# Kernel optimization log

Measured on AMD Instinct MI355X. Metric: run time of the kernel, lower is better.

The kernel has to match this reference:

```python
import jax, jax.numpy as jnp
import numpy as np

DIM = 512
NUM_HEADS = 8
DIM_HEAD = 64
EPS = 1e-8
ROPE_THETA = 10000.0


def rms_norm(x, gamma):
    # F.normalize(x, dim=-1, p=2, eps) * sqrt(dim) * gamma
    norm = jnp.sqrt(jnp.sum(x * x, axis=-1, keepdims=True))
    x = x / jnp.maximum(norm, EPS)
    return x * (DIM ** 0.5) * gamma


def apply_rope(x):
    # x: [b, h, n, d], interleaved-pair RoPE (rotary-embedding-torch style)
    n, d = x.shape[-2], x.shape[-1]
    inv_freq = 1.0 / (ROPE_THETA ** (jnp.arange(0, d, 2, dtype=jnp.float32) / d))
    freqs = jnp.arange(n, dtype=jnp.float32)[:, None] * inv_freq[None, :]  # [n, d/2]
    freqs = jnp.repeat(freqs, 2, axis=-1)  # [n, d]
    cos, sin = jnp.cos(freqs), jnp.sin(freqs)
    x1 = x[..., ::2]
    x2 = x[..., 1::2]
    rot = jnp.stack((-x2, x1), axis=-1).reshape(x.shape)
    return x * cos + rot * sin


def setup_inputs() -> dict:
    key = jax.random.key(0)
    k1, k2, k3, k4 = jax.random.split(key, 4)
    b, n = 4, 2048
    dim_inner = NUM_HEADS * DIM_HEAD
    x = jax.random.normal(k1, (b, n, DIM), dtype=jnp.float32)
    gamma = jnp.ones((DIM,), dtype=jnp.float32)
    w_qkv = jax.random.normal(k2, (DIM, 3 * dim_inner), dtype=jnp.float32) * (DIM ** -0.5)
    w_out = jax.random.normal(k3, (dim_inner, DIM), dtype=jnp.float32) * (dim_inner ** -0.5)
    return {"x": x, "gamma": gamma, "w_qkv": w_qkv, "w_out": w_out}


def reference(x, gamma, w_qkv, w_out):
    b, n, _ = x.shape
    h, d = NUM_HEADS, DIM_HEAD
    xn = rms_norm(x, gamma)
    qkv = xn @ w_qkv  # [b, n, 3*h*d]
    qkv = qkv.reshape(b, n, 3, h, d)
    q = jnp.transpose(qkv[:, :, 0], (0, 2, 1, 3))  # [b, h, n, d]
    k = jnp.transpose(qkv[:, :, 1], (0, 2, 1, 3))
    v = jnp.transpose(qkv[:, :, 2], (0, 2, 1, 3))
    q = apply_rope(q)
    k = apply_rope(k)
    scale = d ** -0.5
    attn = jnp.einsum('bhnd,bhmd->bhnm', q, k) * scale
    attn = jax.nn.softmax(attn, axis=-1)
    out = jnp.einsum('bhnm,bhmd->bhnd', attn, v)
    out = jnp.transpose(out, (0, 2, 1, 3)).reshape(b, n, h * d)
    return out @ w_out
```

## Files before the change

### kernel.cpp

```cpp
#include <hip/hip_runtime.h>
#include <hip/hip_bf16.h>
#include <cmath>

#define B_SZ 4
#define N_SEQ 2048
#define DIM 512
#define NH 8
#define DH 64
#define QKV_N 1536
#define ROWS (B_SZ * N_SEQ)

typedef __bf16 bf16x8 __attribute__((ext_vector_type(8)));
typedef __bf16 bf16x4 __attribute__((ext_vector_type(4)));
typedef float  f32x4  __attribute__((ext_vector_type(4)));

#define GLOAD_LDS16(gp, lp)                                                     \
    __builtin_amdgcn_global_load_lds(                                           \
        (const __attribute__((address_space(1))) void*)(gp),                    \
        (__attribute__((address_space(3))) void*)(lp), 16, 0, 0)

#define MFMA_BF16 __builtin_amdgcn_mfma_f32_16x16x32_bf16

__global__ __launch_bounds__(64) void rmscast_kernel(const float* __restrict__ x,
                                                     const float* __restrict__ gamma,
                                                     __bf16* __restrict__ A) {
    int row = blockIdx.x;
    int t = threadIdx.x;
    const float4* xr = (const float4*)(x + (size_t)row * DIM);
    float4 a = xr[t];
    float4 b = xr[t + 64];
    float ss = a.x*a.x + a.y*a.y + a.z*a.z + a.w*a.w
             + b.x*b.x + b.y*b.y + b.z*b.z + b.w*b.w;
    #pragma unroll
    for (int off = 32; off > 0; off >>= 1) ss += __shfl_xor(ss, off, 64);
    float s = 22.62741699796952f / fmaxf(sqrtf(ss), 1e-8f);
    const float4* gr = (const float4*)gamma;
    float4 g1 = gr[t], g2 = gr[t + 64];
    bf16x4 o1 = { (__bf16)(a.x*g1.x*s), (__bf16)(a.y*g1.y*s),
                  (__bf16)(a.z*g1.z*s), (__bf16)(a.w*g1.w*s) };
    bf16x4 o2 = { (__bf16)(b.x*g2.x*s), (__bf16)(b.y*g2.y*s),
                  (__bf16)(b.z*g2.z*s), (__bf16)(b.w*g2.w*s) };
    *(bf16x4*)(A + (size_t)row * DIM + t * 4)       = o1;
    *(bf16x4*)(A + (size_t)row * DIM + 256 + t * 4) = o2;
}

__global__ __launch_bounds__(256) void tcast_kernel(const float* __restrict__ W,
                                                    __bf16* __restrict__ Wt,
                                                    int K, int N) {
    __shared__ float Ls[64][68];
    const int n0 = blockIdx.x * 64, k0 = blockIdx.y * 64;
    const int t = threadIdx.x, tx = t & 15, ty = t >> 4;
    #pragma unroll
    for (int i = 0; i < 4; i++) {
        int k = ty + i * 16;
        float4 v = *(const float4*)&W[(size_t)(k0 + k) * N + n0 + tx * 4];
        *(float4*)&Ls[k][tx * 4] = v;
    }
    __syncthreads();
    const int nrow = t >> 2, seg = (t & 3) * 16;
    bf16x8 o0, o1;
    #pragma unroll
    for (int j = 0; j < 8; j++) o0[j] = (__bf16)Ls[seg + j][nrow];
    #pragma unroll
    for (int j = 0; j < 8; j++) o1[j] = (__bf16)Ls[seg + 8 + j][nrow];
    *(bf16x8*)&Wt[(size_t)(n0 + nrow) * K + k0 + seg]     = o0;
    *(bf16x8*)&Wt[(size_t)(n0 + nrow) * K + k0 + seg + 8] = o1;
}

template <int N, typename OutT>
__global__ __launch_bounds__(256) void gemm_bf16_kernel(const __bf16* __restrict__ A,
                                                        const __bf16* __restrict__ Bt,
                                                        OutT* __restrict__ C) {
    __shared__ __bf16 As[128 * 32];
    __shared__ __bf16 Bs[128 * 32];
    const int t = threadIdx.x;
    const int lane = t & 63;
    const int w = t >> 6;
    const int l16 = lane & 15, quad = lane >> 4;
    const int wr = w >> 1, wc = w & 1;
    const int row0 = blockIdx.y * 128, col0 = blockIdx.x * 128;

    f32x4 acc[4][4] = {};

    const int r0a = t >> 2,         ks0 = (t & 3) * 8;
    const int r1a = (t + 256) >> 2, ks1 = (t & 3) * 8;

    for (int kt = 0; kt < DIM; kt += 32) {
        __syncthreads();
        GLOAD_LDS16(A  + (size_t)(row0 + r0a) * DIM + kt + ks0, As + t * 8);
        GLOAD_LDS16(A  + (size_t)(row0 + r1a) * DIM + kt + ks1, As + (t + 256) * 8);
        GLOAD_LDS16(Bt + (size_t)(col0 + r0a) * DIM + kt + ks0, Bs + t * 8);
        GLOAD_LDS16(Bt + (size_t)(col0 + r1a) * DIM + kt + ks1, Bs + (t + 256) * 8);
        __syncthreads();
        bf16x8 af[4], bfr[4];
        #pragma unroll
        for (int mi = 0; mi < 4; mi++)
            af[mi] = *(const bf16x8*)(As + (wr * 64 + mi * 16 + l16) * 32 + quad * 8);
        #pragma unroll
        for (int ni = 0; ni < 4; ni++)
            bfr[ni] = *(const bf16x8*)(Bs + (wc * 64 + ni * 16 + l16) * 32 + quad * 8);
        #pragma unroll
        for (int mi = 0; mi < 4; mi++)
            #pragma unroll
            for (int ni = 0; ni < 4; ni++)
                acc[mi][ni] = MFMA_BF16(af[mi], bfr[ni], acc[mi][ni], 0, 0, 0);
    }
    #pragma unroll
    for (int mi = 0; mi < 4; mi++) {
        #pragma unroll
        for (int ni = 0; ni < 4; ni++) {
            #pragma unroll
            for (int r = 0; r < 4; r++) {
                int m = row0 + wr * 64 + mi * 16 + quad * 4 + r;
                int n = col0 + wc * 64 + ni * 16 + l16;
                if constexpr (sizeof(OutT) == 4) {
                    C[(size_t)m * N + n] = acc[mi][ni][r];
                } else {
                    C[(size_t)m * N + n] = (__bf16)acc[mi][ni][r];
                }
            }
        }
    }
}

__global__ __launch_bounds__(256) void prep_kernel(const __bf16* __restrict__ qkvb,
                                                   __bf16* __restrict__ Qb,
                                                   __bf16* __restrict__ Kf,
                                                   __bf16* __restrict__ Vf) {
    const int bx = blockIdx.x;
    const int nt = bx & 31;
    const int bh = bx >> 5;
    const int b  = bh >> 3;
    const int h  = bh & 7;
    const int t  = threadIdx.x;

    {
        const int r  = t >> 2;
        const int d0 = (t & 3) << 4;
        const int pos = nt * 64 + r;
        const __bf16* qp = qkvb + (size_t)(b * N_SEQ + pos) * QKV_N + h * DH + d0;

        union Pack { __bf16 h[16]; uint4 u[2]; };
        Pack qi, ki, qo, ko;
        qi.u[0] = ((const uint4*)qp)[0];         qi.u[1] = ((const uint4*)qp)[1];
        ki.u[0] = ((const uint4*)(qp + 512))[0]; ki.u[1] = ((const uint4*)(qp + 512))[1];

        #pragma unroll
        for (int i = 0; i < 8; i++) {
            int p = (d0 >> 1) + i;
            float inv = exp2f(-0.41524101186092028f * (float)p);
            float ang = (float)pos * inv;
            float sn, cs;
            sincosf(ang, &sn, &cs);
            float qe = (float)qi.h[2*i], qd = (float)qi.h[2*i+1];
            float ke = (float)ki.h[2*i], kd = (float)ki.h[2*i+1];
            qo.h[2*i]   = (__bf16)(0.125f * (qe * cs - qd * sn));
            qo.h[2*i+1] = (__bf16)(0.125f * (qd * cs + qe * sn));
            ko.h[2*i]   = (__bf16)(ke * cs - kd * sn);
            ko.h[2*i+1] = (__bf16)(kd * cs + ke * sn);
        }
        uint4* qd_ = (uint4*)(Qb + ((size_t)bh * N_SEQ + pos) * DH + d0);
        qd_[0] = qo.u[0]; qd_[1] = qo.u[1];
        const int group = r >> 4, kl = r & 15;
        const int c = d0 >> 5, quad = (d0 & 31) >> 3;
        __bf16* kdst = Kf + ((size_t)bh * 32 + nt) * 4096
                          + (group * 2 + c) * 512 + (quad * 16 + kl) * 8;
        *(uint4*)kdst         = ko.u[0];
        *(uint4*)(kdst + 128) = ko.u[1];
    }

    {
        const int w = t >> 6, lane = t & 63;
        union Pack { __bf16 h[16]; uint4 u[2]; };
        Pack v;
        #pragma unroll
        for (int j = 0; j < 16; j++) {
            int row = nt * 64 + w * 16 + j;
            v.h[j] = qkvb[(size_t)(b * N_SEQ + row) * QKV_N + 1024 + h * DH + lane];
        }
        const int ng = lane >> 4, vl = lane & 15;
        __bf16* vdst = Vf + ((size_t)bh * 32 + nt) * 4096
                          + (ng * 2 + (w >> 1)) * 512 + (((w & 1) * 2) * 16 + vl) * 8;
        *(uint4*)vdst         = v.u[0];
        *(uint4*)(vdst + 128) = v.u[1];
    }
}

__global__ __launch_bounds__(256, 2) void attn_mfma_kernel(const __bf16* __restrict__ Qb,
                                                           const __bf16* __restrict__ Kf,
                                                           const __bf16* __restrict__ Vf,
                                                           __bf16* __restrict__ attn) {
    __shared__ __bf16 kv[2][8192];
    __shared__ __bf16 plds[4][2][16][68];

    const int t    = threadIdx.x;
    const int w    = t >> 6;
    const int lane = t & 63;
    const int l16  = lane & 15;
    const int quad = lane >> 4;

    const int bx = blockIdx.x;
    const int bh = bx & 31;
    const int qc = bx >> 5;
    const int b  = bh >> 3;
    const int h  = bh & 7;

    const int qrow = qc * 128 + w * 32;
    const __bf16* Qh = Qb + ((size_t)bh * N_SEQ + qrow) * DH;
    const __bf16* Kt = Kf + (size_t)bh * 32 * 4096;
    const __bf16* Vt = Vf + (size_t)bh * 32 * 4096;

    bf16x8 qa[2][2];
    #pragma unroll
    for (int f = 0; f < 2; f++) {
        qa[f][0] = *(const bf16x8*)(Qh + (size_t)(f * 16 + l16) * DH + quad * 8);
        qa[f][1] = *(const bf16x8*)(Qh + (size_t)(f * 16 + l16) * DH + 32 + quad * 8);
    }

    bf16x8 ones;
    #pragma unroll
    for (int i = 0; i < 8; i++) ones[i] = (__bf16)1.0f;

    f32x4 O[2][4] = {};
    f32x4 L[2] = {};

    auto dma_tile = [&](int tt, int bb) {
        const __bf16* ks = Kt + (size_t)tt * 4096;
        const __bf16* vs = Vt + (size_t)tt * 4096;
        GLOAD_LDS16(ks + w * 512 + lane * 8,       &kv[bb][w * 512 + lane * 8]);
        GLOAD_LDS16(ks + (w + 4) * 512 + lane * 8, &kv[bb][(w + 4) * 512 + lane * 8]);
        GLOAD_LDS16(vs + w * 512 + lane * 8,       &kv[bb][4096 + w * 512 + lane * 8]);
        GLOAD_LDS16(vs + (w + 4) * 512 + lane * 8, &kv[bb][4096 + (w + 4) * 512 + lane * 8]);
    };

    dma_tile(0, 0);
    for (int tt = 0; tt < 32; tt++) {
        const int cur = tt & 1;
        __syncthreads();
        if (tt + 1 < 32) {
            dma_tile(tt + 1, cur ^ 1);
            asm volatile("s_waitcnt vmcnt(4)" ::: "memory");
        } else {
            asm volatile("s_waitcnt vmcnt(0)" ::: "memory");
        }
        __syncthreads();

        const __bf16* kb = kv[cur];
        const __bf16* vb = kv[cur] + 4096;

        bf16x8 kf[4][2];
        #pragma unroll
        for (int g = 0; g < 4; g++)
            #pragma unroll
            for (int c = 0; c < 2; c++)
                kf[g][c] = *(const bf16x8*)(kb + (g * 2 + c) * 512 + lane * 8);
        bf16x8 vf[4][2];
        #pragma unroll
        for (int n = 0; n < 4; n++)
            #pragma unroll
            for (int kc = 0; kc < 2; kc++)
                vf[n][kc] = *(const bf16x8*)(vb + (n * 2 + kc) * 512 + lane * 8);

        #pragma unroll
        for (int f = 0; f < 2; f++) {
            f32x4 S[4];
            #pragma unroll
            for (int g = 0; g < 4; g++) {
                f32x4 z = {0, 0, 0, 0};
                z = MFMA_BF16(qa[f][0], kf[g][0], z, 0, 0, 0);
                z = MFMA_BF16(qa[f][1], kf[g][1], z, 0, 0, 0);
                S[g] = z;
            }
            #pragma unroll
            for (int g = 0; g < 4; g++)
                #pragma unroll
                for (int r = 0; r < 4; r++)
                    plds[w][f][quad * 4 + r][g * 16 + l16] = (__bf16)__expf(S[g][r]);
        }
        asm volatile("s_waitcnt lgkmcnt(0)" ::: "memory");
        #pragma unroll
        for (int f = 0; f < 2; f++) {
            bf16x8 pa0 = *(const bf16x8*)&plds[w][f][l16][quad * 8];
            bf16x8 pa1 = *(const bf16x8*)&plds[w][f][l16][32 + quad * 8];
            #pragma unroll
            for (int n = 0; n < 4; n++) {
                O[f][n] = MFMA_BF16(pa0, vf[n][0], O[f][n], 0, 0, 0);
                O[f][n] = MFMA_BF16(pa1, vf[n][1], O[f][n], 0, 0, 0);
            }
            L[f] = MFMA_BF16(pa0, ones, L[f], 0, 0, 0);
            L[f] = MFMA_BF16(pa1, ones, L[f], 0, 0, 0);
        }
    }

    #pragma unroll
    for (int f = 0; f < 2; f++) {
        float inv[4];
        #pragma unroll
        for (int r = 0; r < 4; r++) inv[r] = 1.0f / L[f][r];
        #pragma unroll
        for (int n = 0; n < 4; n++)
            #pragma unroll
            for (int r = 0; r < 4; r++) {
                size_t row = (size_t)(b * N_SEQ + qrow + f * 16 + quad * 4 + r);
                attn[row * 512 + h * DH + n * 16 + l16] = (__bf16)(O[f][n][r] * inv[r]);
            }
    }
}

extern "C" void kernel_launch(void* const* d_in, const int* in_sizes, int n_in,
                              void* d_out, int out_size, void* d_ws, size_t ws_size,
                              hipStream_t stream) {
    const float* x     = (const float*)d_in[0];
    const float* gamma = (const float*)d_in[1];
    const float* w_qkv = (const float*)d_in[2];
    const float* w_out = (const float*)d_in[3];
    float* out = (float*)d_out;

    __bf16* Abf   = (__bf16*)d_ws;
    __bf16* Wqkvt = Abf + (size_t)ROWS * DIM;
    __bf16* Woutt = Wqkvt + (size_t)QKV_N * DIM;
    __bf16* qkvb  = Woutt + (size_t)DIM * DIM;
    __bf16* attnb = qkvb;
    __bf16* Qb    = qkvb + (size_t)ROWS * QKV_N;
    __bf16* Kf    = Qb + (size_t)NH * B_SZ * N_SEQ * DH;
    __bf16* Vf    = Kf + (size_t)NH * B_SZ * N_SEQ * DH;

    rmscast_kernel<<<ROWS, 64, 0, stream>>>(x, gamma, Abf);
    tcast_kernel<<<dim3(QKV_N / 64, DIM / 64), 256, 0, stream>>>(w_qkv, Wqkvt, DIM, QKV_N);
    tcast_kernel<<<dim3(DIM / 64, DIM / 64), 256, 0, stream>>>(w_out, Woutt, DIM, DIM);
    gemm_bf16_kernel<QKV_N, __bf16><<<dim3(QKV_N / 128, ROWS / 128), 256, 0, stream>>>(
        Abf, Wqkvt, qkvb);
    prep_kernel<<<1024, 256, 0, stream>>>(qkvb, Qb, Kf, Vf);
    attn_mfma_kernel<<<512, 256, 0, stream>>>(Qb, Kf, Vf, attnb);
    gemm_bf16_kernel<DIM, float><<<dim3(DIM / 128, ROWS / 128), 256, 0, stream>>>(
        attnb, Woutt, out);
}
```

Baseline: 179.9 us.

## Split attention KV range across two blocks with atomic fp32 reduction

Each attention block now processes half of the key/value tiles, doubling the grid to 1024 blocks. Partial unnormalized outputs and row sums are combined with fp32 atomicAdd into zeroed buffers, and a new normalize kernel writes the bf16 result. The launch-bounds occupancy hint goes from 2 to 3 blocks per CU. RoPE cos/sin values are precomputed into a table by a small kernel instead of calling sincos inside prep. This trades better CU fill for extra memsets, atomic traffic, a 16MB fp32 intermediate and an extra kernel launch.

```diff
diff --git a/kernel.cpp b/kernel.cpp
--- a/kernel.cpp
+++ b/kernel.cpp
@@ -20,6 +20,15 @@
         (__attribute__((address_space(3))) void*)(lp), 16, 0, 0)
 
 #define MFMA_BF16 __builtin_amdgcn_mfma_f32_16x16x32_bf16
+
+__global__ __launch_bounds__(256) void cs_kernel(float2* __restrict__ cs) {
+    int idx = blockIdx.x * 256 + threadIdx.x;
+    int pos = idx >> 5, p = idx & 31;
+    float ang = (float)pos * exp2f(-0.41524101186092028f * (float)p);
+    float sn, c;
+    sincosf(ang, &sn, &c);
+    cs[idx] = make_float2(c, sn);
+}
 
 __global__ __launch_bounds__(64) void rmscast_kernel(const float* __restrict__ x,
                                                      const float* __restrict__ gamma,
@@ -124,6 +133,7 @@
 }
 
 __global__ __launch_bounds__(256) void prep_kernel(const __bf16* __restrict__ qkvb,
+                                                   const float2* __restrict__ cstab,
                                                    __bf16* __restrict__ Qb,
                                                    __bf16* __restrict__ Kf,
                                                    __bf16* __restrict__ Vf) {
@@ -145,13 +155,11 @@
         qi.u[0] = ((const uint4*)qp)[0];         qi.u[1] = ((const uint4*)qp)[1];
         ki.u[0] = ((const uint4*)(qp + 512))[0]; ki.u[1] = ((const uint4*)(qp + 512))[1];
 
+        const float2* cse = cstab + (size_t)pos * 32 + (t & 3) * 8;
         #pragma unroll
         for (int i = 0; i < 8; i++) {
-            int p = (d0 >> 1) + i;
-            float inv = exp2f(-0.41524101186092028f * (float)p);
-            float ang = (float)pos * inv;
-            float sn, cs;
-            sincosf(ang, &sn, &cs);
+            float2 csv = cse[i];
+            float cs = csv.x, sn = csv.y;
             float qe = (float)qi.h[2*i], qd = (float)qi.h[2*i+1];
             float ke = (float)ki.h[2*i], kd = (float)ki.h[2*i+1];
             qo.h[2*i]   = (__bf16)(0.125f * (qe * cs - qd * sn));
@@ -186,10 +194,11 @@
     }
 }
 
-__global__ __launch_bounds__(256, 2) void attn_mfma_kernel(const __bf16* __restrict__ Qb,
+__global__ __launch_bounds__(256, 3) void attn_mfma_kernel(const __bf16* __restrict__ Qb,
                                                            const __bf16* __restrict__ Kf,
                                                            const __bf16* __restrict__ Vf,
-                                                           __bf16* __restrict__ attn) {
+                                                           float* __restrict__ Opart,
+                                                           float* __restrict__ Lb) {
     __shared__ __bf16 kv[2][8192];
     __shared__ __bf16 plds[4][2][16][68];
 
@@ -201,14 +210,15 @@
 
     const int bx = blockIdx.x;
     const int bh = bx & 31;
-    const int qc = bx >> 5;
+    const int ks = (bx >> 5) & 1;
+    const int qc = bx >> 6;
     const int b  = bh >> 3;
     const int h  = bh & 7;
 
     const int qrow = qc * 128 + w * 32;
     const __bf16* Qh = Qb + ((size_t)bh * N_SEQ + qrow) * DH;
-    const __bf16* Kt = Kf + (size_t)bh * 32 * 4096;
-    const __bf16* Vt = Vf + (size_t)bh * 32 * 4096;
+    const __bf16* Kt = Kf + ((size_t)bh * 32 + ks * 16) * 4096;
+    const __bf16* Vt = Vf + ((size_t)bh * 32 + ks * 16) * 4096;
 
     bf16x8 qa[2][2];
     #pragma unroll
@@ -225,19 +235,19 @@
     f32x4 L[2] = {};
 
     auto dma_tile = [&](int tt, int bb) {
-        const __bf16* ks = Kt + (size_t)tt * 4096;
-        const __bf16* vs = Vt + (size_t)tt * 4096;
-        GLOAD_LDS16(ks + w * 512 + lane * 8,       &kv[bb][w * 512 + lane * 8]);
-        GLOAD_LDS16(ks + (w + 4) * 512 + lane * 8, &kv[bb][(w + 4) * 512 + lane * 8]);
-        GLOAD_LDS16(vs + w * 512 + lane * 8,       &kv[bb][4096 + w * 512 + lane * 8]);
-        GLOAD_LDS16(vs + (w + 4) * 512 + lane * 8, &kv[bb][4096 + (w + 4) * 512 + lane * 8]);
+        const __bf16* kss = Kt + (size_t)tt * 4096;
+        const __bf16* vss = Vt + (size_t)tt * 4096;
+        GLOAD_LDS16(kss + w * 512 + lane * 8,       &kv[bb][w * 512 + lane * 8]);
+        GLOAD_LDS16(kss + (w + 4) * 512 + lane * 8, &kv[bb][(w + 4) * 512 + lane * 8]);
+        GLOAD_LDS16(vss + w * 512 + lane * 8,       &kv[bb][4096 + w * 512 + lane * 8]);
+        GLOAD_LDS16(vss + (w + 4) * 512 + lane * 8, &kv[bb][4096 + (w + 4) * 512 + lane * 8]);
     };
 
     dma_tile(0, 0);
-    for (int tt = 0; tt < 32; tt++) {
+    for (int tt = 0; tt < 16; tt++) {
         const int cur = tt & 1;
         __syncthreads();
-        if (tt + 1 < 32) {
+        if (tt + 1 < 16) {
             dma_tile(tt + 1, cur ^ 1);
             asm volatile("s_waitcnt vmcnt(4)" ::: "memory");
         } else {
@@ -294,17 +304,30 @@
 
     #pragma unroll
     for (int f = 0; f < 2; f++) {
-        float inv[4];
-        #pragma unroll
-        for (int r = 0; r < 4; r++) inv[r] = 1.0f / L[f][r];
-        #pragma unroll
-        for (int n = 0; n < 4; n++)
-            #pragma unroll
-            for (int r = 0; r < 4; r++) {
-                size_t row = (size_t)(b * N_SEQ + qrow + f * 16 + quad * 4 + r);
-                attn[row * 512 + h * DH + n * 16 + l16] = (__bf16)(O[f][n][r] * inv[r]);
-            }
-    }
+        #pragma unroll
+        for (int r = 0; r < 4; r++) {
+            size_t row = (size_t)(b * N_SEQ + qrow + f * 16 + quad * 4 + r);
+            #pragma unroll
+            for (int n = 0; n < 4; n++)
+                atomicAdd(&Opart[row * 512 + h * DH + n * 16 + l16], O[f][n][r]);
+            if (l16 == 0)
+                atomicAdd(&Lb[(size_t)bh * N_SEQ + qrow + f * 16 + quad * 4 + r], L[f][r]);
+        }
+    }
+}
+
+__global__ __launch_bounds__(256) void norm_kernel(const float* __restrict__ Opart,
+                                                   const float* __restrict__ Lb,
+                                                   __bf16* __restrict__ attnb) {
+    int idx = blockIdx.x * 256 + threadIdx.x;
+    int row = idx >> 7, c4 = idx & 127;
+    int h = c4 >> 4;
+    float l = Lb[(size_t)(((row >> 11) << 3) + h) * N_SEQ + (row & (N_SEQ - 1))];
+    float inv = 1.0f / l;
+    float4 o = ((const float4*)Opart)[idx];
+    bf16x4 ob = { (__bf16)(o.x * inv), (__bf16)(o.y * inv),
+                  (__bf16)(o.z * inv), (__bf16)(o.w * inv) };
+    *(bf16x4*)(attnb + (size_t)idx * 4) = ob;
 }
 
 extern "C" void kernel_launch(void* const* d_in, const int* in_sizes, int n_in,
@@ -320,18 +343,26 @@
     __bf16* Wqkvt = Abf + (size_t)ROWS * DIM;
     __bf16* Woutt = Wqkvt + (size_t)QKV_N * DIM;
     __bf16* qkvb  = Woutt + (size_t)DIM * DIM;
-    __bf16* attnb = qkvb;
+    float*  Opart = (float*)qkvb;
+    float*  Lb    = Opart + (size_t)ROWS * 512;
+    __bf16* attnb = Abf;
     __bf16* Qb    = qkvb + (size_t)ROWS * QKV_N;
     __bf16* Kf    = Qb + (size_t)NH * B_SZ * N_SEQ * DH;
     __bf16* Vf    = Kf + (size_t)NH * B_SZ * N_SEQ * DH;
-
+    float2* cstab = (float2*)(Vf + (size_t)NH * B_SZ * N_SEQ * DH);
+
+    cs_kernel<<<256, 256, 0, stream>>>(cstab);
     rmscast_kernel<<<ROWS, 64, 0, stream>>>(x, gamma, Abf);
     tcast_kernel<<<dim3(QKV_N / 64, DIM / 64), 256, 0, stream>>>(w_qkv, Wqkvt, DIM, QKV_N);
     tcast_kernel<<<dim3(DIM / 64, DIM / 64), 256, 0, stream>>>(w_out, Woutt, DIM, DIM);
     gemm_bf16_kernel<QKV_N, __bf16><<<dim3(QKV_N / 128, ROWS / 128), 256, 0, stream>>>(
         Abf, Wqkvt, qkvb);
-    prep_kernel<<<1024, 256, 0, stream>>>(qkvb, Qb, Kf, Vf);
-    attn_mfma_kernel<<<512, 256, 0, stream>>>(Qb, Kf, Vf, attnb);
+    prep_kernel<<<1024, 256, 0, stream>>>(qkvb, cstab, Qb, Kf, Vf);
+    hipMemsetAsync(Opart, 0, ((size_t)ROWS * 512 + ROWS * NH / 2) * sizeof(float) + 0,
+                   stream);
+    hipMemsetAsync(Lb, 0, (size_t)NH * B_SZ * N_SEQ * sizeof(float), stream);
+    attn_mfma_kernel<<<1024, 256, 0, stream>>>(Qb, Kf, Vf, Opart, Lb);
+    norm_kernel<<<ROWS * 128 / 256, 256, 0, stream>>>(Opart, Lb, attnb);
     gemm_bf16_kernel<DIM, float><<<dim3(DIM / 128, ROWS / 128), 256, 0, stream>>>(
         attnb, Woutt, out);
 }
```

Result: slower. 211.6 us (+17.6%).

## Triple-buffer attention K/V tiles, fold log2e into Q scale, merge weight casts

Applied to the files above, without the earlier changes.

The attention loop moves from double to triple buffering of the K/V LDS tiles. It prefetches two tiles ahead and uses a single waitcnt-plus-barrier per iteration instead of two __syncthreads, which cuts synchronisation stalls and hides global-to-LDS latency. The Q scale now folds in log2(e), so the softmax can use exp2f directly instead of __expf. The two weight transpose-cast launches are merged into one kernel to save a launch. The extra K/V buffer raises LDS use per block, which may limit occupancy under the launch bound of 2 blocks.

```diff
diff --git a/kernel.cpp b/kernel.cpp
--- a/kernel.cpp
+++ b/kernel.cpp
@@ -44,12 +44,11 @@
     *(bf16x4*)(A + (size_t)row * DIM + 256 + t * 4) = o2;
 }
 
-__global__ __launch_bounds__(256) void tcast_kernel(const float* __restrict__ W,
-                                                    __bf16* __restrict__ Wt,
-                                                    int K, int N) {
-    __shared__ float Ls[64][68];
-    const int n0 = blockIdx.x * 64, k0 = blockIdx.y * 64;
-    const int t = threadIdx.x, tx = t & 15, ty = t >> 4;
+__device__ __forceinline__ void tcast_tile(const float* __restrict__ W,
+                                           __bf16* __restrict__ Wt,
+                                           int K, int N, int n0, int k0, int t,
+                                           float (*Ls)[68]) {
+    const int tx = t & 15, ty = t >> 4;
     #pragma unroll
     for (int i = 0; i < 4; i++) {
         int k = ty + i * 16;
@@ -65,6 +64,16 @@
     for (int j = 0; j < 8; j++) o1[j] = (__bf16)Ls[seg + 8 + j][nrow];
     *(bf16x8*)&Wt[(size_t)(n0 + nrow) * K + k0 + seg]     = o0;
     *(bf16x8*)&Wt[(size_t)(n0 + nrow) * K + k0 + seg + 8] = o1;
+}
+
+__global__ __launch_bounds__(256) void tcast2_kernel(const float* __restrict__ w_qkv,
+                                                     const float* __restrict__ w_out,
+                                                     __bf16* __restrict__ Wqkvt,
+                                                     __bf16* __restrict__ Woutt) {
+    __shared__ float Ls[64][68];
+    const int bx = blockIdx.x, k0 = blockIdx.y * 64, t = threadIdx.x;
+    if (bx < 24) tcast_tile(w_qkv, Wqkvt, DIM, QKV_N, bx * 64, k0, t, Ls);
+    else         tcast_tile(w_out, Woutt, DIM, DIM, (bx - 24) * 64, k0, t, Ls);
 }
 
 template <int N, typename OutT>
@@ -133,6 +142,7 @@
     const int b  = bh >> 3;
     const int h  = bh & 7;
     const int t  = threadIdx.x;
+    const float QSCALE = 0.18033688011112042f;
 
     {
         const int r  = t >> 2;
@@ -154,8 +164,8 @@
             sincosf(ang, &sn, &cs);
             float qe = (float)qi.h[2*i], qd = (float)qi.h[2*i+1];
             float ke = (float)ki.h[2*i], kd = (float)ki.h[2*i+1];
-            qo.h[2*i]   = (__bf16)(0.125f * (qe * cs - qd * sn));
-            qo.h[2*i+1] = (__bf16)(0.125f * (qd * cs + qe * sn));
+            qo.h[2*i]   = (__bf16)(QSCALE * (qe * cs - qd * sn));
+            qo.h[2*i+1] = (__bf16)(QSCALE * (qd * cs + qe * sn));
             ko.h[2*i]   = (__bf16)(ke * cs - kd * sn);
             ko.h[2*i+1] = (__bf16)(kd * cs + ke * sn);
         }
@@ -190,7 +200,7 @@
                                                            const __bf16* __restrict__ Kf,
                                                            const __bf16* __restrict__ Vf,
                                                            __bf16* __restrict__ attn) {
-    __shared__ __bf16 kv[2][8192];
+    __shared__ __bf16 kv[3][8192];
     __shared__ __bf16 plds[4][2][16][68];
 
     const int t    = threadIdx.x;
@@ -225,25 +235,27 @@
     f32x4 L[2] = {};
 
     auto dma_tile = [&](int tt, int bb) {
-        const __bf16* ks = Kt + (size_t)tt * 4096;
-        const __bf16* vs = Vt + (size_t)tt * 4096;
-        GLOAD_LDS16(ks + w * 512 + lane * 8,       &kv[bb][w * 512 + lane * 8]);
-        GLOAD_LDS16(ks + (w + 4) * 512 + lane * 8, &kv[bb][(w + 4) * 512 + lane * 8]);
-        GLOAD_LDS16(vs + w * 512 + lane * 8,       &kv[bb][4096 + w * 512 + lane * 8]);
-        GLOAD_LDS16(vs + (w + 4) * 512 + lane * 8, &kv[bb][4096 + (w + 4) * 512 + lane * 8]);
+        const __bf16* kss = Kt + (size_t)tt * 4096;
+        const __bf16* vss = Vt + (size_t)tt * 4096;
+        GLOAD_LDS16(kss + w * 512 + lane * 8,       &kv[bb][w * 512 + lane * 8]);
+        GLOAD_LDS16(kss + (w + 4) * 512 + lane * 8, &kv[bb][(w + 4) * 512 + lane * 8]);
+        GLOAD_LDS16(vss + w * 512 + lane * 8,       &kv[bb][4096 + w * 512 + lane * 8]);
+        GLOAD_LDS16(vss + (w + 4) * 512 + lane * 8, &kv[bb][4096 + (w + 4) * 512 + lane * 8]);
     };
 
     dma_tile(0, 0);
+    dma_tile(1, 1);
+    int cur = 0;
+    #pragma unroll 1
     for (int tt = 0; tt < 32; tt++) {
-        const int cur = tt & 1;
-        __syncthreads();
-        if (tt + 1 < 32) {
-            dma_tile(tt + 1, cur ^ 1);
-            asm volatile("s_waitcnt vmcnt(4)" ::: "memory");
-        } else {
-            asm volatile("s_waitcnt vmcnt(0)" ::: "memory");
-        }
-        __syncthreads();
+        if (tt < 31)
+            asm volatile("s_waitcnt vmcnt(4)\n\ts_barrier" ::: "memory");
+        else
+            asm volatile("s_waitcnt vmcnt(0)\n\ts_barrier" ::: "memory");
+        if (tt + 2 < 32) {
+            int pf = cur + 2; if (pf >= 3) pf -= 3;
+            dma_tile(tt + 2, pf);
+        }
 
         const __bf16* kb = kv[cur];
         const __bf16* vb = kv[cur] + 4096;
@@ -275,7 +287,7 @@
             for (int g = 0; g < 4; g++)
                 #pragma unroll
                 for (int r = 0; r < 4; r++)
-                    plds[w][f][quad * 4 + r][g * 16 + l16] = (__bf16)__expf(S[g][r]);
+                    plds[w][f][quad * 4 + r][g * 16 + l16] = (__bf16)exp2f(S[g][r]);
         }
         asm volatile("s_waitcnt lgkmcnt(0)" ::: "memory");
         #pragma unroll
@@ -290,6 +302,7 @@
             L[f] = MFMA_BF16(pa0, ones, L[f], 0, 0, 0);
             L[f] = MFMA_BF16(pa1, ones, L[f], 0, 0, 0);
         }
+        cur = (cur == 2) ? 0 : cur + 1;
     }
 
     #pragma unroll
@@ -326,8 +339,7 @@
     __bf16* Vf    = Kf + (size_t)NH * B_SZ * N_SEQ * DH;
 
     rmscast_kernel<<<ROWS, 64, 0, stream>>>(x, gamma, Abf);
-    tcast_kernel<<<dim3(QKV_N / 64, DIM / 64), 256, 0, stream>>>(w_qkv, Wqkvt, DIM, QKV_N);
-    tcast_kernel<<<dim3(DIM / 64, DIM / 64), 256, 0, stream>>>(w_out, Woutt, DIM, DIM);
+    tcast2_kernel<<<dim3(32, 8), 256, 0, stream>>>(w_qkv, w_out, Wqkvt, Woutt);
     gemm_bf16_kernel<QKV_N, __bf16><<<dim3(QKV_N / 128, ROWS / 128), 256, 0, stream>>>(
         Abf, Wqkvt, qkvb);
     prep_kernel<<<1024, 256, 0, stream>>>(qkvb, Qb, Kf, Vf);
```

Result: slower. 187.7 us (+4.4%).
